# Optimization experiments

Measured on AMD Instinct MI355X. Metric: run time of the kernel, lower is better.

## Reference

```python
import jax, jax.numpy as jnp
import numpy as np

B, S, D = 2, 2048, 1024
H, DK, DV = 16, 64, 64


def setup_inputs() -> dict:
    key = jax.random.key(0)
    ks = jax.random.split(key, 11)
    s = 1.0 / np.sqrt(D)
    inp = {
        "Q": jax.random.normal(ks[0], (B, S, D), jnp.float32),
        "K": jax.random.normal(ks[1], (B, S, D), jnp.float32),
        "V": jax.random.normal(ks[2], (B, S, D), jnp.float32),
        "Wq": jax.random.normal(ks[3], (H, D, DK), jnp.float32) * s,
        "bq": jax.random.normal(ks[4], (H, DK), jnp.float32) * 0.01,
        "Wk": jax.random.normal(ks[5], (H, D, DK), jnp.float32) * s,
        "bk": jax.random.normal(ks[6], (H, DK), jnp.float32) * 0.01,
        "Wv": jax.random.normal(ks[7], (H, D, DV), jnp.float32) * s,
        "bv": jax.random.normal(ks[8], (H, DV), jnp.float32) * 0.01,
        "Wm": jax.random.normal(ks[9], (H * DV, D), jnp.float32) * (1.0 / np.sqrt(H * DV)),
        "bm": jax.random.normal(ks[10], (D,), jnp.float32) * 0.01,
    }
    return inp


def reference(Q, K, V, Wq, bq, Wk, bk, Wv, bv, Wm, bm):
    # Per-head projections (batched over heads instead of a Python loop)
    q = jnp.einsum("bqd,hdk->bhqk", Q, Wq) + bq[None, :, None, :]   # [B,H,S,DK]
    k = jnp.einsum("bsd,hdk->bhsk", K, Wk) + bk[None, :, None, :]   # [B,H,S,DK]
    v = jnp.einsum("bsd,hdv->bhsv", V, Wv) + bv[None, :, None, :]   # [B,H,S,DV]
    scores = jnp.einsum("bhqk,bhsk->bhqs", q, k) / jnp.sqrt(jnp.asarray(DK, q.dtype))
    attn = jax.nn.softmax(scores, axis=-1)                           # [B,H,S,S]
    ctx = jnp.einsum("bhqs,bhsv->bhqv", attn, v)                     # [B,H,S,DV]
    # Concat heads along feature dim, then output projection
    stacked_ctx = jnp.transpose(ctx, (0, 2, 1, 3)).reshape(B, S, H * DV)
    multi_head = stacked_ctx @ Wm + bm                               # [B,S,D]
    # torch.cat(attn_weights_list, dim=-1): [B, S, H*S]
    stacked_attention_weights = jnp.transpose(attn, (0, 2, 1, 3)).reshape(B, S, H * S)
    return multi_head, stacked_attention_weights
```

## Files before the change

kernel.cpp:

```cpp
#include <hip/hip_runtime.h>

#define B_ 2
#define S_ 2048
#define D_ 1024
#define H_ 16
#define M_ 4096

typedef unsigned short u16;
typedef unsigned int u32;
typedef short bf8 __attribute__((ext_vector_type(8)));
typedef float f4 __attribute__((ext_vector_type(4)));

#define MFMA16(a, b, c) __builtin_amdgcn_mfma_f32_16x16x32_bf16(a, b, c, 0, 0, 0)

__device__ __forceinline__ u16 f2b(float f) {
  u32 u = __builtin_bit_cast(u32, f);
  u += 0x7fffu + ((u >> 16) & 1);
  return (u16)(u >> 16);
}
__device__ __forceinline__ u32 pack2(float lo, float hi) {
  return (u32)f2b(lo) | ((u32)f2b(hi) << 16);
}
__device__ __forceinline__ float b2f(u16 h) {
  return __builtin_bit_cast(float, (u32)h << 16);
}
__device__ __forceinline__ bf8 g16(const u16* p) { return *(const bf8*)p; }

__device__ __forceinline__ bf8 ldA(const u16* lds, int rowBase, int kc, int lane) {
  int row = rowBase + (lane & 15);
  int c = (kc * 4 + (lane >> 4)) ^ (row & 7);
  return *(const bf8*)(lds + row * 64 + c * 8);
}

__device__ __forceinline__ void stage_async(u16* ldsdst, const u16* __restrict__ gsrc,
                                            int srcStride, int lane) {
  int row = lane >> 3;
  int c16 = (lane & 7) ^ (row & 7);
  const u16* g = gsrc + (size_t)row * srcStride + c16 * 8;
  __builtin_amdgcn_global_load_lds((const __attribute__((address_space(1))) void*)g,
                                   (__attribute__((address_space(3))) void*)ldsdst,
                                   16, 0, 0);
}

__device__ __forceinline__ void stageB(u16* lds, const u16* __restrict__ src,
                                       int srcStride, int t) {
#pragma unroll
  for (int i = 0; i < 4; ++i) {
    int c = t + 256 * i;
    int row = c >> 3, col = c & 7;
    uint4 v = *(const uint4*)(src + (size_t)row * srcStride + col * 8);
    *(uint4*)(lds + row * 64 + (col ^ (row & 7)) * 8) = v;
  }
}

__device__ __forceinline__ void stageAf(u16* lds, const float* __restrict__ src,
                                        int srcStride, int t) {
#pragma unroll
  for (int i = 0; i < 4; ++i) {
    int c = t + 256 * i;
    int row = c >> 3, col = c & 7;
    const float* p = src + (size_t)row * srcStride + col * 8;
    float4 a = *(const float4*)p;
    float4 b = *(const float4*)(p + 4);
    uint4 o;
    o.x = pack2(a.x, a.y);
    o.y = pack2(a.z, a.w);
    o.z = pack2(b.x, b.y);
    o.w = pack2(b.z, b.w);
    *(uint4*)(lds + row * 64 + (col ^ (row & 7)) * 8) = o;
  }
}

__global__ __launch_bounds__(256) void tcvt(const float* __restrict__ in,
                                            u16* __restrict__ out, int R, int C) {
  int rt = blockIdx.x, ct = blockIdx.y, z = blockIdx.z;
  in += (size_t)z * R * C;
  out += (size_t)z * R * C;
  __shared__ float tile[64][65];
  int t = threadIdx.x;
  int r = t >> 2, cc = (t & 3) * 16;
#pragma unroll
  for (int j = 0; j < 16; j += 4) {
    float4 v = *(const float4*)(in + (size_t)(rt * 64 + r) * C + ct * 64 + cc + j);
    tile[r][cc + j] = v.x;
    tile[r][cc + j + 1] = v.y;
    tile[r][cc + j + 2] = v.z;
    tile[r][cc + j + 3] = v.w;
  }
  __syncthreads();
  int c = t >> 2;
  u32 buf[8];
#pragma unroll
  for (int j = 0; j < 8; ++j)
    buf[j] = pack2(tile[cc + 2 * j][c], tile[cc + 2 * j + 1][c]);
  uint4* dst = (uint4*)(out + (size_t)(ct * 64 + c) * R + rt * 64 + cc);
  dst[0] = make_uint4(buf[0], buf[1], buf[2], buf[3]);
  dst[1] = make_uint4(buf[4], buf[5], buf[6], buf[7]);
}

__global__ __launch_bounds__(256) void tcvt3(const float* __restrict__ Wq,
                                             const float* __restrict__ Wk,
                                             const float* __restrict__ Wv,
                                             u16* __restrict__ WT0,
                                             u16* __restrict__ WT1,
                                             u16* __restrict__ WT2) {
  int rt = blockIdx.x, z = blockIdx.z;
  int mat = z >> 4, hh = z & 15;
  const float* in = (mat == 0 ? Wq : mat == 1 ? Wk : Wv) + (size_t)hh * 1024 * 64;
  u16* out = (mat == 0 ? WT0 : mat == 1 ? WT1 : WT2) + (size_t)hh * 1024 * 64;
  __shared__ float tile[64][65];
  int t = threadIdx.x;
  int r = t >> 2, cc = (t & 3) * 16;
#pragma unroll
  for (int j = 0; j < 16; j += 4) {
    float4 v = *(const float4*)(in + (size_t)(rt * 64 + r) * 64 + cc + j);
    tile[r][cc + j] = v.x;
    tile[r][cc + j + 1] = v.y;
    tile[r][cc + j + 2] = v.z;
    tile[r][cc + j + 3] = v.w;
  }
  __syncthreads();
  int c = t >> 2;
  u32 buf[8];
#pragma unroll
  for (int j = 0; j < 8; ++j)
    buf[j] = pack2(tile[cc + 2 * j][c], tile[cc + 2 * j + 1][c]);
  uint4* dst = (uint4*)(out + (size_t)c * 1024 + rt * 64 + cc);
  dst[0] = make_uint4(buf[0], buf[1], buf[2], buf[3]);
  dst[1] = make_uint4(buf[4], buf[5], buf[6], buf[7]);
}

__global__ __launch_bounds__(256) void proj3(
    const float* __restrict__ Qf, const float* __restrict__ Kf,
    const float* __restrict__ Vf, const u16* __restrict__ WT0,
    const u16* __restrict__ WT1, const u16* __restrict__ WT2,
    const float* __restrict__ bq, const float* __restrict__ bk,
    const float* __restrict__ bv, u16* __restrict__ qp, u16* __restrict__ kp,
    u16* __restrict__ vTp) {
  int mt = blockIdx.x, nt = blockIdx.y, z = blockIdx.z;
  const float* Ap = z == 0 ? Qf : z == 1 ? Kf : Vf;
  const u16* BT = z == 0 ? WT0 : z == 1 ? WT1 : WT2;
  const float* bias = z == 0 ? bq : z == 1 ? bk : bv;
  float scale = z == 0 ? 0.125f : 1.0f;
  int t = threadIdx.x, lane = t & 63, w = t >> 6;
  int wr = w >> 1, wc = w & 1;
  int quad = lane >> 4, col = lane & 15;
  __shared__ u16 Asm[128 * 64], Bsm[128 * 64];
  f4 acc[4][4] = {};
  for (int kt = 0; kt < 16; ++kt) {
    __syncthreads();
    stageAf(Asm, Ap + (size_t)(mt * 128) * 1024 + kt * 64, 1024, t);
    stageB(Bsm, BT + (size_t)(nt * 128) * 1024 + kt * 64, 1024, t);
    __syncthreads();
#pragma unroll
    for (int kc = 0; kc < 2; ++kc) {
      bf8 a[4], b[4];
#pragma unroll
      for (int fr = 0; fr < 4; ++fr) a[fr] = ldA(Asm, wr * 64 + fr * 16, kc, lane);
#pragma unroll
      for (int nf = 0; nf < 4; ++nf) b[nf] = ldA(Bsm, wc * 64 + nf * 16, kc, lane);
#pragma unroll
      for (int fr = 0; fr < 4; ++fr)
#pragma unroll
        for (int nf = 0; nf < 4; ++nf)
          acc[fr][nf] = MFMA16(a[fr], b[nf], acc[fr][nf]);
    }
  }
  if (z < 2) {
    u16* outp = z == 0 ? qp : kp;
#pragma unroll
    for (int fr = 0; fr < 4; ++fr)
#pragma unroll
      for (int nf = 0; nf < 4; ++nf) {
        int n = nt * 128 + wc * 64 + nf * 16 + col;
        int h = n >> 6, d = n & 63;
        float bs = bias[n];
#pragma unroll
        for (int r = 0; r < 4; ++r) {
          int gm = mt * 128 + wr * 64 + fr * 16 + quad * 4 + r;
          int bb = gm >> 11, s = gm & 2047;
          outp[(size_t)((bb * H_ + h) * S_ + s) * 64 + d] =
              f2b((acc[fr][nf][r] + bs) * scale);
        }
      }
  } else {
#pragma unroll
    for (int fr = 0; fr < 4; ++fr)
#pragma unroll
      for (int nf = 0; nf < 4; ++nf) {
        int n = nt * 128 + wc * 64 + nf * 16 + col;
        int h = n >> 6, d = n & 63;
        float bs = bias[n];
        int s0 = mt * 128 + wr * 64 + fr * 16 + quad * 4;
        int bb = s0 >> 11, s = s0 & 2047;
        uint2 u;
        u.x = pack2(acc[fr][nf][0] + bs, acc[fr][nf][1] + bs);
        u.y = pack2(acc[fr][nf][2] + bs, acc[fr][nf][3] + bs);
        *(uint2*)(vTp + (size_t)((bb * H_ + h) * 64 + d) * S_ + s) = u;
      }
  }
}

__global__ __launch_bounds__(256) void gemmo(const u16* __restrict__ A,
                                             const u16* __restrict__ BT,
                                             const float* __restrict__ bias,
                                             float* __restrict__ outp) {
  int mt = blockIdx.x, nt = blockIdx.y;
  int t = threadIdx.x, lane = t & 63, w = t >> 6;
  int wr = w >> 1, wc = w & 1;
  int quad = lane >> 4, col = lane & 15;
  __shared__ u16 Asm[128 * 64], Bsm[128 * 64];
  f4 acc[4][4] = {};
  for (int kt = 0; kt < 16; ++kt) {
    __syncthreads();
    stageB(Asm, A + (size_t)(mt * 128) * 1024 + kt * 64, 1024, t);
    stageB(Bsm, BT + (size_t)(nt * 128) * 1024 + kt * 64, 1024, t);
    __syncthreads();
#pragma unroll
    for (int kc = 0; kc < 2; ++kc) {
      bf8 a[4], b[4];
#pragma unroll
      for (int fr = 0; fr < 4; ++fr) a[fr] = ldA(Asm, wr * 64 + fr * 16, kc, lane);
#pragma unroll
      for (int nf = 0; nf < 4; ++nf) b[nf] = ldA(Bsm, wc * 64 + nf * 16, kc, lane);
#pragma unroll
      for (int fr = 0; fr < 4; ++fr)
#pragma unroll
        for (int nf = 0; nf < 4; ++nf)
          acc[fr][nf] = MFMA16(a[fr], b[nf], acc[fr][nf]);
    }
  }
#pragma unroll
  for (int fr = 0; fr < 4; ++fr)
#pragma unroll
    for (int nf = 0; nf < 4; ++nf) {
      int n = nt * 128 + wc * 64 + nf * 16 + col;
      float bs = bias[n];
#pragma unroll
      for (int r = 0; r < 4; ++r) {
        int gm = mt * 128 + wr * 64 + fr * 16 + quad * 4 + r;
        outp[(size_t)gm * 1024 + n] = acc[fr][nf][r] + bs;
      }
    }
}

__global__ void attn6(const u16* __restrict__ qp, const u16* __restrict__ kp,
                      const u16* __restrict__ vT, u16* __restrict__ ctxo,
                      float* __restrict__ attw) {
  int bid = blockIdx.x;
  int l = (bid & 7) * 128 + (bid >> 3);
  int qt = l & 31, hb = l >> 5;
  int h = hb & 15, b = hb >> 4;
  int t = threadIdx.x, lane = t & 63, w = t >> 6;
  int quad = lane >> 4, col = lane & 15;

  __shared__ u16 KV[4][64 * 64];
  __shared__ u16 Psm[4][16 * 64];

  const u16* kbase = kp + (size_t)(b * H_ + h) * S_ * 64;
  const u16* vbase = vT + (size_t)(b * H_ + h) * 64 * S_;
  const u16* qrow = qp + ((size_t)(b * H_ + h) * S_ + qt * 64 + w * 16) * 64;
  int r16 = (lane & 15) * 64;
  int c0 = (lane >> 4) * 8, c1 = c0 + 32;
  bf8 qf0 = g16(qrow + r16 + c0);
  bf8 qf1 = g16(qrow + r16 + c1);

#define SLOT(i) (KV[0] + (size_t)((i) & 3) * 4096)
#define SGT(slot, kt)                                                             \
  {                                                                               \
    u16* s_ = (slot);                                                             \
    const u16* g_ = kbase + (size_t)((kt) & 31) * 4096;                           \
    stage_async(s_ + w * 1024, g_ + w * 16 * 64, 64, lane);                       \
    stage_async(s_ + w * 1024 + 512, g_ + (w * 16 + 8) * 64, 64, lane);           \
  }
#define SGV(bi, kt)                                                               \
  {                                                                               \
    u16* s_ = KV[2 + (bi)];                                                       \
    stage_async(s_ + w * 1024, vbase + (size_t)(w * 16) * S_ + (kt) * 64, S_,     \
                lane);                                                            \
    stage_async(s_ + w * 1024 + 512,                                              \
                vbase + (size_t)(w * 16 + 8) * S_ + (kt) * 64, S_, lane);         \
  }
#define WAITVM(N)                                          \
  asm volatile("s_waitcnt vmcnt(" #N ")" ::: "memory");    \
  __builtin_amdgcn_sched_barrier(0)
#define BAR()                      \
  __builtin_amdgcn_s_barrier();    \
  __builtin_amdgcn_sched_barrier(0)

  SGT(SLOT(0), 0);
  SGT(SLOT(1), 1);
  WAITVM(2);
  BAR();
  float lsum = 0.f;
  for (int kt = 0; kt < 32; ++kt) {
    SGT(SLOT(kt + 2), kt + 2);
    WAITVM(4);
    BAR();
    const u16* Kc = SLOT(kt);
    f4 sc[4] = {};
#pragma unroll
    for (int fr = 0; fr < 4; ++fr) {
      bf8 k0 = ldA(Kc, fr * 16, 0, lane);
      bf8 k1 = ldA(Kc, fr * 16, 1, lane);
      sc[fr] = MFMA16(k0, qf0, sc[fr]);
      sc[fr] = MFMA16(k1, qf1, sc[fr]);
    }
    float s = 0.f;
#pragma unroll
    for (int fr = 0; fr < 4; ++fr)
#pragma unroll
      for (int r = 0; r < 4; ++r) s += __expf(sc[fr][r]);
    lsum += s;
  }
  lsum += __shfl_xor(lsum, 16);
  lsum += __shfl_xor(lsum, 32);
  float linv = 1.f / lsum;

  BAR();
  SGV(0, 0);
  WAITVM(0);
  BAR();
  f4 ctxa[4] = {};
  u16* Pw = Psm[w];
  size_t awrow = ((size_t)(b * S_ + qt * 64 + w * 16) * H_ + h) * S_;
  for (int kt = 0; kt < 32; ++kt) {
    SGT(SLOT((kt + 1) & 1), kt + 1);
    SGV((kt + 1) & 1, (kt + 1) & 31);
    const u16* Kc = SLOT(kt & 1);
    const u16* Vc = KV[2 + (kt & 1)];
    f4 sc[4] = {};
#pragma unroll
    for (int fr = 0; fr < 4; ++fr) {
      bf8 k0 = ldA(Kc, fr * 16, 0, lane);
      bf8 k1 = ldA(Kc, fr * 16, 1, lane);
      sc[fr] = MFMA16(k0, qf0, sc[fr]);
      sc[fr] = MFMA16(k1, qf1, sc[fr]);
    }
#pragma unroll
    for (int fr = 0; fr < 4; ++fr) {
      float p0 = __expf(sc[fr][0]) * linv;
      float p1 = __expf(sc[fr][1]) * linv;
      float p2 = __expf(sc[fr][2]) * linv;
      float p3 = __expf(sc[fr][3]) * linv;
      int bo = col * 128 + ((fr * 32 + quad * 8) ^ ((col & 7) << 4));
      uint2 u;
      u.x = pack2(p0, p1);
      u.y = pack2(p2, p3);
      *(uint2*)((char*)Pw + bo) = u;
    }
#pragma unroll
    for (int it = 0; it < 2; ++it) {
      int row = (lane >> 3) + 8 * it;
      int cc = lane & 7;
      int bo = row * 128 + ((cc ^ (row & 7)) << 4);
      bf8 pv = *(const bf8*)((const char*)Pw + bo);
      float* dst = attw + awrow + (size_t)row * (H_ * S_) + kt * 64 + cc * 8;
      float4 o0, o1;
      o0.x = b2f((u16)pv[0]);
      o0.y = b2f((u16)pv[1]);
      o0.z = b2f((u16)pv[2]);
      o0.w = b2f((u16)pv[3]);
      o1.x = b2f((u16)pv[4]);
      o1.y = b2f((u16)pv[5]);
      o1.z = b2f((u16)pv[6]);
      o1.w = b2f((u16)pv[7]);
      *(float4*)dst = o0;
      *((float4*)dst + 1) = o1;
    }
    bf8 pf0 = ldA(Pw, 0, 0, lane);
    bf8 pf1 = ldA(Pw, 0, 1, lane);
#pragma unroll
    for (int fr = 0; fr < 4; ++fr) {
      bf8 v0 = ldA(Vc, fr * 16, 0, lane);
      bf8 v1 = ldA(Vc, fr * 16, 1, lane);
      ctxa[fr] = MFMA16(v0, pf0, ctxa[fr]);
      ctxa[fr] = MFMA16(v1, pf1, ctxa[fr]);
    }
    WAITVM(8);
    BAR();
  }
  int qg = qt * 64 + w * 16 + col;
  size_t cb = ((size_t)(b * S_ + qg) * H_ + h) * 64;
#pragma unroll
  for (int fr = 0; fr < 4; ++fr) {
    uint2 u;
    u.x = pack2(ctxa[fr][0], ctxa[fr][1]);
    u.y = pack2(ctxa[fr][2], ctxa[fr][3]);
    *(uint2*)(ctxo + cb + fr * 16 + quad * 4) = u;
  }
#undef SLOT
#undef SGT
#undef SGV
#undef WAITVM
#undef BAR
}

extern "C" void kernel_launch(void* const* d_in, const int* in_sizes, int n_in,
                              void* d_out, int out_size, void* d_ws, size_t ws_size,
                              hipStream_t stream) {
  const float* Q = (const float*)d_in[0];
  const float* K = (const float*)d_in[1];
  const float* V = (const float*)d_in[2];
  const float* Wq = (const float*)d_in[3];
  const float* bq = (const float*)d_in[4];
  const float* Wk = (const float*)d_in[5];
  const float* bk = (const float*)d_in[6];
  const float* Wv = (const float*)d_in[7];
  const float* bv = (const float*)d_in[8];
  const float* Wm = (const float*)d_in[9];
  const float* bm = (const float*)d_in[10];
  float* out0 = (float*)d_out;
  float* out1 = out0 + (size_t)M_ * D_;
  (void)in_sizes; (void)n_in; (void)out_size; (void)ws_size;

  u16* WT0 = (u16*)d_ws;
  u16* WT1 = WT0 + 1048576;
  u16* WT2 = WT1 + 1048576;
  u16* WT3 = WT2 + 1048576;
  u16* qp = WT3 + 1048576;
  u16* kp = qp + 4194304;
  u16* ctx = kp + 4194304;
  u16* vTp = ctx + 4194304;

  tcvt3<<<dim3(16, 1, 48), 256, 0, stream>>>(Wq, Wk, Wv, WT0, WT1, WT2);
  tcvt<<<dim3(16, 16, 1), 256, 0, stream>>>(Wm, WT3, 1024, 1024);
  proj3<<<dim3(32, 8, 3), 256, 0, stream>>>(Q, K, V, WT0, WT1, WT2, bq, bk, bv,
                                            qp, kp, vTp);
  attn6<<<1024, 256, 0, stream>>>(qp, kp, vTp, ctx, out1);
  gemmo<<<dim3(32, 8), 256, 0, stream>>>(ctx, WT3, bm, out0);
}
```

Measured before the change: 296.4 us.

## Pre-convert activations to bf16 and double-buffer projection GEMMs with async LDS loads

Adds a separate kernel that converts Q, K and V from fp32 to bf16 up front. The projection and output GEMMs now use double-buffered LDS tiles filled by async global-to-LDS loads, so the next K-tile loads while the current one is computed. The attention kernel's in-loop wait count is tightened from 8 to 4. The cost is an extra launch and an extra round trip of activation traffic through the workspace, with the ctx buffer reused as scratch for the converted Q.

```diff
diff --git a/kernel.cpp b/kernel.cpp
--- a/kernel.cpp
+++ b/kernel.cpp
@@ -42,33 +42,31 @@
                                    16, 0, 0);
 }
 
-__device__ __forceinline__ void stageB(u16* lds, const u16* __restrict__ src,
-                                       int srcStride, int t) {
-#pragma unroll
-  for (int i = 0; i < 4; ++i) {
-    int c = t + 256 * i;
-    int row = c >> 3, col = c & 7;
-    uint4 v = *(const uint4*)(src + (size_t)row * srcStride + col * 8);
-    *(uint4*)(lds + row * 64 + (col ^ (row & 7)) * 8) = v;
-  }
-}
-
-__device__ __forceinline__ void stageAf(u16* lds, const float* __restrict__ src,
-                                        int srcStride, int t) {
-#pragma unroll
-  for (int i = 0; i < 4; ++i) {
-    int c = t + 256 * i;
-    int row = c >> 3, col = c & 7;
-    const float* p = src + (size_t)row * srcStride + col * 8;
-    float4 a = *(const float4*)p;
-    float4 b = *(const float4*)(p + 4);
-    uint4 o;
-    o.x = pack2(a.x, a.y);
-    o.y = pack2(a.z, a.w);
-    o.z = pack2(b.x, b.y);
-    o.w = pack2(b.z, b.w);
-    *(uint4*)(lds + row * 64 + (col ^ (row & 7)) * 8) = o;
-  }
+#define WAITVM(N)                                          \
+  asm volatile("s_waitcnt vmcnt(" #N ")" ::: "memory");    \
+  __builtin_amdgcn_sched_barrier(0)
+#define BAR()                      \
+  __builtin_amdgcn_s_barrier();    \
+  __builtin_amdgcn_sched_barrier(0)
+
+__global__ __launch_bounds__(256) void cvtk3(const float* __restrict__ Q,
+                                             const float* __restrict__ K,
+                                             const float* __restrict__ V,
+                                             u16* __restrict__ Xq,
+                                             u16* __restrict__ Xk,
+                                             u16* __restrict__ Xv) {
+  int z = blockIdx.z;
+  const float* in = z == 0 ? Q : z == 1 ? K : V;
+  u16* out = z == 0 ? Xq : z == 1 ? Xk : Xv;
+  int i = (blockIdx.x * 256 + threadIdx.x) * 8;
+  float4 a = *(const float4*)(in + i);
+  float4 b = *(const float4*)(in + i + 4);
+  uint4 o;
+  o.x = pack2(a.x, a.y);
+  o.y = pack2(a.z, a.w);
+  o.z = pack2(b.x, b.y);
+  o.w = pack2(b.z, b.w);
+  *(uint4*)(out + i) = o;
 }
 
 __global__ __launch_bounds__(256) void tcvt(const float* __restrict__ in,
@@ -130,42 +128,60 @@
   dst[1] = make_uint4(buf[4], buf[5], buf[6], buf[7]);
 }
 
-__global__ __launch_bounds__(256) void proj3(
-    const float* __restrict__ Qf, const float* __restrict__ Kf,
-    const float* __restrict__ Vf, const u16* __restrict__ WT0,
+__global__ __launch_bounds__(256) void proj4(
+    const u16* __restrict__ Xq, const u16* __restrict__ Xk,
+    const u16* __restrict__ Xv, const u16* __restrict__ WT0,
     const u16* __restrict__ WT1, const u16* __restrict__ WT2,
     const float* __restrict__ bq, const float* __restrict__ bk,
     const float* __restrict__ bv, u16* __restrict__ qp, u16* __restrict__ kp,
     u16* __restrict__ vTp) {
   int mt = blockIdx.x, nt = blockIdx.y, z = blockIdx.z;
-  const float* Ap = z == 0 ? Qf : z == 1 ? Kf : Vf;
+  const u16* Ap = z == 0 ? Xq : z == 1 ? Xk : Xv;
   const u16* BT = z == 0 ? WT0 : z == 1 ? WT1 : WT2;
   const float* bias = z == 0 ? bq : z == 1 ? bk : bv;
   float scale = z == 0 ? 0.125f : 1.0f;
   int t = threadIdx.x, lane = t & 63, w = t >> 6;
   int wr = w >> 1, wc = w & 1;
   int quad = lane >> 4, col = lane & 15;
-  __shared__ u16 Asm[128 * 64], Bsm[128 * 64];
+  __shared__ u16 Asm[2][128 * 64], Bsm[2][128 * 64];
+
+#define PSTG(bi, kt)                                                            \
+  {                                                                             \
+    _Pragma("unroll") for (int cc_ = 0; cc_ < 4; ++cc_) {                       \
+      int rb_ = w * 32 + cc_ * 8;                                               \
+      stage_async(Asm[bi] + rb_ * 64,                                           \
+                  Ap + (size_t)(mt * 128 + rb_) * 1024 + (kt) * 64, 1024, lane);\
+      stage_async(Bsm[bi] + rb_ * 64,                                           \
+                  BT + (size_t)(nt * 128 + rb_) * 1024 + (kt) * 64, 1024, lane);\
+    }                                                                           \
+  }
+
   f4 acc[4][4] = {};
+  PSTG(0, 0);
+  WAITVM(0);
+  BAR();
   for (int kt = 0; kt < 16; ++kt) {
-    __syncthreads();
-    stageAf(Asm, Ap + (size_t)(mt * 128) * 1024 + kt * 64, 1024, t);
-    stageB(Bsm, BT + (size_t)(nt * 128) * 1024 + kt * 64, 1024, t);
-    __syncthreads();
+    int bi = kt & 1;
+    if (kt < 15) PSTG(bi ^ 1, kt + 1);
 #pragma unroll
     for (int kc = 0; kc < 2; ++kc) {
       bf8 a[4], b[4];
 #pragma unroll
-      for (int fr = 0; fr < 4; ++fr) a[fr] = ldA(Asm, wr * 64 + fr * 16, kc, lane);
-#pragma unroll
-      for (int nf = 0; nf < 4; ++nf) b[nf] = ldA(Bsm, wc * 64 + nf * 16, kc, lane);
+      for (int fr = 0; fr < 4; ++fr) a[fr] = ldA(Asm[bi], wr * 64 + fr * 16, kc, lane);
+#pragma unroll
+      for (int nf = 0; nf < 4; ++nf) b[nf] = ldA(Bsm[bi], wc * 64 + nf * 16, kc, lane);
 #pragma unroll
       for (int fr = 0; fr < 4; ++fr)
 #pragma unroll
         for (int nf = 0; nf < 4; ++nf)
           acc[fr][nf] = MFMA16(a[fr], b[nf], acc[fr][nf]);
     }
-  }
+    if (kt < 15) {
+      WAITVM(0);
+      BAR();
+    }
+  }
+#undef PSTG
   if (z < 2) {
     u16* outp = z == 0 ? qp : kp;
 #pragma unroll
@@ -201,35 +217,53 @@
   }
 }
 
-__global__ __launch_bounds__(256) void gemmo(const u16* __restrict__ A,
-                                             const u16* __restrict__ BT,
-                                             const float* __restrict__ bias,
-                                             float* __restrict__ outp) {
+__global__ __launch_bounds__(256) void gemmo2(const u16* __restrict__ A,
+                                              const u16* __restrict__ BT,
+                                              const float* __restrict__ bias,
+                                              float* __restrict__ outp) {
   int mt = blockIdx.x, nt = blockIdx.y;
   int t = threadIdx.x, lane = t & 63, w = t >> 6;
   int wr = w >> 1, wc = w & 1;
   int quad = lane >> 4, col = lane & 15;
-  __shared__ u16 Asm[128 * 64], Bsm[128 * 64];
+  __shared__ u16 Asm[2][128 * 64], Bsm[2][128 * 64];
+
+#define PSTG(bi, kt)                                                            \
+  {                                                                             \
+    _Pragma("unroll") for (int cc_ = 0; cc_ < 4; ++cc_) {                       \
+      int rb_ = w * 32 + cc_ * 8;                                               \
+      stage_async(Asm[bi] + rb_ * 64,                                           \
+                  A + (size_t)(mt * 128 + rb_) * 1024 + (kt) * 64, 1024, lane); \
+      stage_async(Bsm[bi] + rb_ * 64,                                           \
+                  BT + (size_t)(nt * 128 + rb_) * 1024 + (kt) * 64, 1024, lane);\
+    }                                                                           \
+  }
+
   f4 acc[4][4] = {};
+  PSTG(0, 0);
+  WAITVM(0);
+  BAR();
   for (int kt = 0; kt < 16; ++kt) {
-    __syncthreads();
-    stageB(Asm, A + (size_t)(mt * 128) * 1024 + kt * 64, 1024, t);
-    stageB(Bsm, BT + (size_t)(nt * 128) * 1024 + kt * 64, 1024, t);
-    __syncthreads();
+    int bi = kt & 1;
+    if (kt < 15) PSTG(bi ^ 1, kt + 1);
 #pragma unroll
     for (int kc = 0; kc < 2; ++kc) {
       bf8 a[4], b[4];
 #pragma unroll
-      for (int fr = 0; fr < 4; ++fr) a[fr] = ldA(Asm, wr * 64 + fr * 16, kc, lane);
-#pragma unroll
-      for (int nf = 0; nf < 4; ++nf) b[nf] = ldA(Bsm, wc * 64 + nf * 16, kc, lane);
+      for (int fr = 0; fr < 4; ++fr) a[fr] = ldA(Asm[bi], wr * 64 + fr * 16, kc, lane);
+#pragma unroll
+      for (int nf = 0; nf < 4; ++nf) b[nf] = ldA(Bsm[bi], wc * 64 + nf * 16, kc, lane);
 #pragma unroll
       for (int fr = 0; fr < 4; ++fr)
 #pragma unroll
         for (int nf = 0; nf < 4; ++nf)
           acc[fr][nf] = MFMA16(a[fr], b[nf], acc[fr][nf]);
     }
-  }
+    if (kt < 15) {
+      WAITVM(0);
+      BAR();
+    }
+  }
+#undef PSTG
 #pragma unroll
   for (int fr = 0; fr < 4; ++fr)
 #pragma unroll
@@ -244,7 +278,7 @@
     }
 }
 
-__global__ void attn6(const u16* __restrict__ qp, const u16* __restrict__ kp,
+__global__ void attn7(const u16* __restrict__ qp, const u16* __restrict__ kp,
                       const u16* __restrict__ vT, u16* __restrict__ ctxo,
                       float* __restrict__ attw) {
   int bid = blockIdx.x;
@@ -281,12 +315,6 @@
     stage_async(s_ + w * 1024 + 512,                                              \
                 vbase + (size_t)(w * 16 + 8) * S_ + (kt) * 64, S_, lane);         \
   }
-#define WAITVM(N)                                          \
-  asm volatile("s_waitcnt vmcnt(" #N ")" ::: "memory");    \
-  __builtin_amdgcn_sched_barrier(0)
-#define BAR()                      \
-  __builtin_amdgcn_s_barrier();    \
-  __builtin_amdgcn_sched_barrier(0)
 
   SGT(SLOT(0), 0);
   SGT(SLOT(1), 1);
@@ -377,7 +405,7 @@
       ctxa[fr] = MFMA16(v0, pf0, ctxa[fr]);
       ctxa[fr] = MFMA16(v1, pf1, ctxa[fr]);
     }
-    WAITVM(8);
+    WAITVM(4);
     BAR();
   }
   int qg = qt * 64 + w * 16 + col;
@@ -392,8 +420,6 @@
 #undef SLOT
 #undef SGT
 #undef SGV
-#undef WAITVM
-#undef BAR
 }
 
 extern "C" void kernel_launch(void* const* d_in, const int* in_sizes, int n_in,
@@ -420,13 +446,16 @@
   u16* WT3 = WT2 + 1048576;
   u16* qp = WT3 + 1048576;
   u16* kp = qp + 4194304;
-  u16* ctx = kp + 4194304;
-  u16* vTp = ctx + 4194304;
-
+  u16* vTp = kp + 4194304;
+  u16* ctx = vTp + 4194304;
+  u16* Xk = ctx + 4194304;
+  u16* Xv = Xk + 4194304;
+
+  cvtk3<<<dim3(2048, 1, 3), 256, 0, stream>>>(Q, K, V, ctx, Xk, Xv);
   tcvt3<<<dim3(16, 1, 48), 256, 0, stream>>>(Wq, Wk, Wv, WT0, WT1, WT2);
   tcvt<<<dim3(16, 16, 1), 256, 0, stream>>>(Wm, WT3, 1024, 1024);
-  proj3<<<dim3(32, 8, 3), 256, 0, stream>>>(Q, K, V, WT0, WT1, WT2, bq, bk, bv,
-                                            qp, kp, vTp);
-  attn6<<<1024, 256, 0, stream>>>(qp, kp, vTp, ctx, out1);
-  gemmo<<<dim3(32, 8), 256, 0, stream>>>(ctx, WT3, bm, out0);
-}
+  proj4<<<dim3(32, 8, 3), 256, 0, stream>>>(ctx, Xk, Xv, WT0, WT1, WT2, bq, bk,
+                                            bv, qp, kp, vTp);
+  attn7<<<1024, 256, 0, stream>>>(qp, kp, vTp, ctx, out1);
+  gemmo2<<<dim3(32, 8), 256, 0, stream>>>(ctx, WT3, bm, out0);
+}
```

Measured after the change: 288.3 us. 1.03x faster.
